# Optimization experiments

Hardware: AMD Instinct MI355X
Metric: run time of the kernel (lower is better)

The kernel has to match this reference:

```python
import jax, jax.numpy as jnp
import numpy as np

EPS = 1e-06
N_HEADS = 32
HEAD_DIM = 128
D_STATE = 128
D_MODEL = 2048
D_INNER = 4096
BATCH = 64


def setup_inputs() -> dict:
    key = jax.random.key(0)
    ks = jax.random.split(key, 8)
    bc_dim = N_HEADS * D_STATE
    theta_dim = N_HEADS * (D_STATE // 2)
    proj_dim = 2 * D_INNER + 2 * bc_dim + 2 * N_HEADS + theta_dim  # 18496
    x = jax.random.normal(ks[0], (BATCH, D_MODEL), jnp.float32)
    h = jax.random.normal(ks[1], (BATCH, N_HEADS, D_STATE, HEAD_DIM), jnp.float32) * 0.1
    B_prev = jax.random.normal(ks[2], (BATCH, N_HEADS, D_STATE), jnp.float32)
    x_prev = jax.random.normal(ks[3], (BATCH, N_HEADS, HEAD_DIM), jnp.float32)
    theta_cumsum = jax.random.normal(ks[4], (BATCH, N_HEADS, D_STATE // 2), jnp.float32)
    W_in = jax.random.normal(ks[5], (proj_dim, D_MODEL), jnp.float32) * 0.02
    # A_log initialized as log(arange(1, d_state+1)) repeated per head
    A_log = jnp.log(jnp.arange(1, D_STATE + 1, dtype=jnp.float32))[None, :].repeat(N_HEADS, axis=0)
    B_bias = jnp.ones((N_HEADS, D_STATE), jnp.float32)
    C_bias = jnp.ones((N_HEADS, D_STATE), jnp.float32)
    W_out = jax.random.normal(ks[6], (D_MODEL, D_INNER), jnp.float32) * 0.02
    return {"x": x, "h": h, "B_prev": B_prev, "x_prev": x_prev,
            "theta_cumsum": theta_cumsum, "W_in": W_in, "A_log": A_log,
            "B_bias": B_bias, "C_bias": C_bias, "W_out": W_out}


def _rms_norm(v):
    # RMS over last dim (v already fp32)
    rms = jnp.sqrt(jnp.mean(v * v, axis=-1, keepdims=True) + EPS)
    return v / rms


def _apply_rope(v, freqs):
    # v: (B,H,N), freqs: (B,H,N//2); interleaved pairs
    vp = v.reshape(*v.shape[:-1], -1, 2)
    c, s = jnp.cos(freqs), jnp.sin(freqs)
    v0, v1 = vp[..., 0], vp[..., 1]
    y0 = v0 * c - v1 * s
    y1 = v0 * s + v1 * c
    return jnp.stack([y0, y1], axis=-1).reshape(v.shape)


def reference(x, h, B_prev, x_prev, theta_cumsum, W_in, A_log, B_bias, C_bias, W_out):
    batch = x.shape[0]
    bc_dim = N_HEADS * D_STATE
    proj = x @ W_in.T  # (B, proj_dim)
    idx = 0
    x_proj = proj[:, idx:idx + D_INNER]; idx += D_INNER
    z = proj[:, idx:idx + D_INNER]; idx += D_INNER
    B_raw = proj[:, idx:idx + bc_dim]; idx += bc_dim
    C_raw = proj[:, idx:idx + bc_dim]; idx += bc_dim
    dt_raw = proj[:, idx:idx + N_HEADS]; idx += N_HEADS
    lam_raw = proj[:, idx:idx + N_HEADS]; idx += N_HEADS
    theta = proj[:, idx:].reshape(batch, N_HEADS, D_STATE // 2)

    x_proj = x_proj.reshape(batch, N_HEADS, HEAD_DIM)
    z = z.reshape(batch, N_HEADS, HEAD_DIM)
    B_raw = B_raw.reshape(batch, N_HEADS, D_STATE)
    C_raw = C_raw.reshape(batch, N_HEADS, D_STATE)

    B = _rms_norm(B_raw) + B_bias
    C = _rms_norm(C_raw) + C_bias

    dt = jax.nn.softplus(dt_raw)                       # (B,H)
    theta_cumsum_new = theta_cumsum + theta * dt[:, :, None]
    B = _apply_rope(B, theta_cumsum_new)
    C = _apply_rope(C, theta_cumsum_new)

    lam = jax.nn.sigmoid(lam_raw)                      # (B,H)
    A = -jnp.mean(jnp.exp(A_log), axis=-1)             # (H,)
    alpha = jnp.exp(dt * A)                            # (B,H)
    beta = (1.0 - lam) * dt * alpha
    gamma = lam * dt

    Bx_prev = jnp.einsum('bhn,bhp->bhnp', B_prev, x_prev)
    Bx_curr = jnp.einsum('bhn,bhp->bhnp', B, x_proj)
    h_new = (alpha[:, :, None, None] * h
             + beta[:, :, None, None] * Bx_prev
             + gamma[:, :, None, None] * Bx_curr)      # (B,H,N,P)

    y = jnp.einsum('bhn,bhnp->bhp', C, h_new)
    y = y * jax.nn.silu(z)
    y = y.reshape(batch, D_INNER) @ W_out.T            # (B, d_model)
    return y, h_new, B, x_proj, theta_cumsum_new
```

## Files before the change

### kernel.cpp

```cpp
#include <hip/hip_runtime.h>
#include <hip/hip_bf16.h>
#include <cstdint>
#include <cmath>

#define EPSV 1e-6f
#define PSTR 1183744

typedef __attribute__((ext_vector_type(8))) short bf16x8;
typedef __attribute__((ext_vector_type(4))) float f32x4;

typedef __attribute__((address_space(3))) unsigned int lds_u32;
typedef const __attribute__((address_space(1))) unsigned int g_u32;

__device__ __forceinline__ void load_lds16(const void* g, void* l) {
  __builtin_amdgcn_global_load_lds((g_u32*)g, (lds_u32*)l, 16, 0, 0);
}

__device__ __forceinline__ short f2b(float f) {
  unsigned u = __float_as_uint(f);
  u = (u + 0x7fffu + ((u >> 16) & 1u)) >> 16;
  return (short)u;
}

__device__ __forceinline__ bf16x8 cvt8(float4 a, float4 b) {
  bf16x8 v;
  v[0]=f2b(a.x); v[1]=f2b(a.y); v[2]=f2b(a.z); v[3]=f2b(a.w);
  v[4]=f2b(b.x); v[5]=f2b(b.y); v[6]=f2b(b.z); v[7]=f2b(b.w);
  return v;
}

__global__ __launch_bounds__(256) void conv_bf16(
    const float* __restrict__ in, short* __restrict__ out, int n8) {
  const int i = blockIdx.x * 256 + threadIdx.x;
  if (i < n8) {
    float4 a = ((const float4*)in)[2 * i];
    float4 b = ((const float4*)in)[2 * i + 1];
    ((bf16x8*)out)[i] = cvt8(a, b);
  }
}

template<int KSPLIT, int NT>
__global__ __launch_bounds__(256, 2) void gemm_wlds(
    const short* __restrict__ Abf, const float* __restrict__ W,
    float* __restrict__ Outp, int N, int K) {
  __shared__ float Wlds[3][64 * 64];
  __shared__ short Alds[3][64 * 64];
  const int tid = threadIdx.x;
  const int lane = tid & 63;
  const int wv = tid >> 6;
  const int lrow = lane & 15, lk = lane >> 4;
  const int bid = blockIdx.x;
  const int ks = bid % KSPLIT;
  const int nblk = (bid / KSPLIT) * 64;
  const int kbase = ks * (NT * 64);

  f32x4 acc[4];
#pragma unroll
  for (int i = 0; i < 4; ++i) acc[i] = (f32x4){0.f, 0.f, 0.f, 0.f};

  auto stage = [&](int buf, int k0) {
#pragma unroll
    for (int j = 0; j < 4; ++j) {
      const int c = wv * 4 + j;
      const int r = c * 4 + (lane >> 4);
      const int g = (lane & 15) ^ (r & 15);
      load_lds16(W + (size_t)(nblk + r) * K + k0 + g * 4,
                 (char*)&Wlds[buf][0] + c * 1024);
    }
#pragma unroll
    for (int j = 0; j < 2; ++j) {
      const int c = wv * 2 + j;
      const int r = c * 8 + (lane >> 3);
      const int g = (lane & 7) ^ (r & 7);
      load_lds16(Abf + (size_t)r * K + k0 + g * 8,
                 (char*)&Alds[buf][0] + c * 1024);
    }
  };

  auto compute = [&](int buf) {
    const int wr = wv * 16 + lrow;
#pragma unroll
    for (int kc = 0; kc < 2; ++kc) {
      const int g0 = kc * 8 + lk * 2;
      const float4 wlo = *(const float4*)((const char*)&Wlds[buf][0]
                          + wr * 256 + ((g0 ^ (lrow & 15)) * 16));
      const float4 whi = *(const float4*)((const char*)&Wlds[buf][0]
                          + wr * 256 + (((g0 + 1) ^ (lrow & 15)) * 16));
      const bf16x8 wb = cvt8(wlo, whi);
#pragma unroll
      for (int mf = 0; mf < 4; ++mf) {
        const int ar = mf * 16 + lrow;
        const int ga = ((kc << 2) | lk) ^ (ar & 7);
        const bf16x8 av = *(const bf16x8*)((const char*)&Alds[buf][0]
                           + ar * 128 + ga * 16);
        acc[mf] = __builtin_amdgcn_mfma_f32_16x16x32_bf16(av, wb, acc[mf], 0, 0, 0);
      }
    }
  };

  stage(0, kbase);
  stage(1, kbase + 64);

  for (int t = 0; t < NT; ++t) {
    if (t < NT - 1) asm volatile("s_waitcnt vmcnt(6)" ::: "memory");
    else            asm volatile("s_waitcnt vmcnt(0)" ::: "memory");
    __builtin_amdgcn_sched_barrier(0);
    __builtin_amdgcn_s_barrier();
    __builtin_amdgcn_sched_barrier(0);
    compute(t % 3);
    if (t + 2 <= NT - 1) stage((t + 2) % 3, kbase + (t + 2) * 64);
  }

  float* ob = Outp + (size_t)ks * 64 * N + nblk + wv * 16 + lrow;
#pragma unroll
  for (int mf = 0; mf < 4; ++mf)
#pragma unroll
    for (int i = 0; i < 4; ++i)
      ob[(size_t)(mf * 16 + lk * 4 + i) * N] = acc[mf][i];
}

__device__ __forceinline__ float block_reduce_sum256(float v, float* red, int t) {
#pragma unroll
  for (int o = 32; o > 0; o >>= 1) v += __shfl_xor(v, o, 64);
  __syncthreads();
  if ((t & 63) == 0) red[t >> 6] = v;
  __syncthreads();
  return red[0] + red[1] + red[2] + red[3];
}

__global__ __launch_bounds__(256) void state_update(
    const float* __restrict__ pp, const float* __restrict__ h,
    const float* __restrict__ B_prev, const float* __restrict__ x_prev,
    const float* __restrict__ theta_cumsum, const float* __restrict__ A_log,
    const float* __restrict__ B_bias, const float* __restrict__ C_bias,
    float* __restrict__ o_h, float* __restrict__ o_B,
    float* __restrict__ o_xp, float* __restrict__ o_th,
    short* __restrict__ ysbf) {
  const int bid = blockIdx.x;
  const int b = bid >> 5, hd = bid & 31;
  const int t = threadIdx.x;
  const size_t pb = (size_t)b * 18496;
#define PJ(o) (pp[pb + (o)] + pp[PSTR + pb + (o)] + pp[2 * PSTR + pb + (o)] \
             + pp[3 * PSTR + pb + (o)])

  __shared__ float sB[128], sC[128], sBp[128], sXp[128], sXv[128];
  __shared__ float red[8];
  __shared__ float yred[8][128];

  float aval = (t < 128) ? expf(A_log[hd * 128 + t]) : 0.f;
  float brv  = (t < 128) ? PJ(8192 + hd * 128 + t) : 0.f;
  float crv  = (t < 128) ? PJ(12288 + hd * 128 + t) : 0.f;
  if (t < 128) {
    sBp[t] = B_prev[(size_t)bid * 128 + t];
    float xp = PJ(hd * 128 + t);
    sXp[t] = xp;
    o_xp[(size_t)bid * 128 + t] = xp;
    sXv[t] = x_prev[(size_t)bid * 128 + t];
  }
  float sumA  = block_reduce_sum256(aval, red, t);
  float sumB2 = block_reduce_sum256(brv * brv, red, t);
  float sumC2 = block_reduce_sum256(crv * crv, red, t);

  const float dt_raw  = PJ(16384 + hd);
  const float lam_raw = PJ(16416 + hd);
  const float dt  = (dt_raw > 20.f) ? dt_raw : log1pf(expf(dt_raw));
  const float lam = 1.f / (1.f + expf(-lam_raw));
  const float A     = -sumA * (1.f / 128.f);
  const float alpha = expf(dt * A);
  const float beta  = (1.f - lam) * dt * alpha;
  const float gamma = lam * dt;
  const float rb = rsqrtf(sumB2 * (1.f / 128.f) + EPSV);
  const float rc = rsqrtf(sumC2 * (1.f / 128.f) + EPSV);

  if (t < 64) {
    float b0 = PJ(8192 + hd * 128 + 2 * t);
    float b1 = PJ(8192 + hd * 128 + 2 * t + 1);
    float c0 = PJ(12288 + hd * 128 + 2 * t);
    float c1 = PJ(12288 + hd * 128 + 2 * t + 1);
    b0 = b0 * rb + B_bias[hd * 128 + 2 * t];
    b1 = b1 * rb + B_bias[hd * 128 + 2 * t + 1];
    c0 = c0 * rc + C_bias[hd * 128 + 2 * t];
    c1 = c1 * rc + C_bias[hd * 128 + 2 * t + 1];
    const float th = theta_cumsum[(size_t)bid * 64 + t]
                   + PJ(16448 + hd * 64 + t) * dt;
    o_th[(size_t)bid * 64 + t] = th;
    const float cth = cosf(th), sth = sinf(th);
    const float nb0 = b0 * cth - b1 * sth, nb1 = b0 * sth + b1 * cth;
    const float nc0 = c0 * cth - c1 * sth, nc1 = c0 * sth + c1 * cth;
    sB[2 * t] = nb0; sB[2 * t + 1] = nb1;
    sC[2 * t] = nc0; sC[2 * t + 1] = nc1;
    o_B[(size_t)bid * 128 + 2 * t] = nb0;
    o_B[(size_t)bid * 128 + 2 * t + 1] = nb1;
  }
  __syncthreads();

  const int p4 = t & 31, nb = t >> 5;
  const float4 xp4 = *(const float4*)&sXp[p4 * 4];
  const float4 xv4 = *(const float4*)&sXv[p4 * 4];
  const size_t hbase = (size_t)bid * 16384;
  float4 ya = {0.f, 0.f, 0.f, 0.f};
  for (int n = nb; n < 128; n += 8) {
    const float4 hv = *(const float4*)&h[hbase + n * 128 + p4 * 4];
    const float cb = gamma * sB[n];
    const float cp = beta * sBp[n];
    float4 hn;
    hn.x = alpha * hv.x + cp * xv4.x + cb * xp4.x;
    hn.y = alpha * hv.y + cp * xv4.y + cb * xp4.y;
    hn.z = alpha * hv.z + cp * xv4.z + cb * xp4.z;
    hn.w = alpha * hv.w + cp * xv4.w + cb * xp4.w;
    *(float4*)&o_h[hbase + n * 128 + p4 * 4] = hn;
    const float cn = sC[n];
    ya.x += cn * hn.x; ya.y += cn * hn.y; ya.z += cn * hn.z; ya.w += cn * hn.w;
  }
  *(float4*)&yred[nb][p4 * 4] = ya;
  __syncthreads();
  if (t < 128) {
    float y = 0.f;
#pragma unroll
    for (int j = 0; j < 8; ++j) y += yred[j][t];
    const float zv = PJ(4096 + hd * 128 + t);
    const float sig = 1.f / (1.f + expf(-zv));
    ysbf[(size_t)b * 4096 + hd * 128 + t] = f2b(y * zv * sig);
  }
#undef PJ
}

__global__ __launch_bounds__(256) void reduce_y(
    const float* __restrict__ yp, float* __restrict__ y, int n4) {
  const int i = blockIdx.x * 256 + threadIdx.x;
  if (i < n4) {
    float4 s = ((const float4*)yp)[i];
#pragma unroll
    for (int k = 1; k < 16; ++k) {
      float4 t = ((const float4*)(yp + (size_t)k * 131072))[i];
      s.x += t.x; s.y += t.y; s.z += t.z; s.w += t.w;
    }
    ((float4*)y)[i] = s;
  }
}

extern "C" void kernel_launch(void* const* d_in, const int* in_sizes, int n_in,
                              void* d_out, int out_size, void* d_ws, size_t ws_size,
                              hipStream_t stream) {
  const float* x            = (const float*)d_in[0];
  const float* h            = (const float*)d_in[1];
  const float* B_prev       = (const float*)d_in[2];
  const float* x_prev       = (const float*)d_in[3];
  const float* theta_cumsum = (const float*)d_in[4];
  const float* W_in         = (const float*)d_in[5];
  const float* A_log        = (const float*)d_in[6];
  const float* B_bias       = (const float*)d_in[7];
  const float* C_bias       = (const float*)d_in[8];
  const float* W_out        = (const float*)d_in[9];

  float* out  = (float*)d_out;
  float* o_y  = out;
  float* o_h  = out + 131072;
  float* o_B  = o_h + 33554432;
  float* o_xp = o_B + 262144;
  float* o_th = o_xp + 262144;

  float* pp   = (float*)d_ws;
  float* yp   = pp;
  short* xbf  = (short*)(pp + 4 * PSTR);
  short* ysbf = xbf + 131072;

  conv_bf16<<<dim3(64), dim3(256), 0, stream>>>(x, xbf, 16384);
  gemm_wlds<4, 8><<<dim3(289 * 4), dim3(256), 0, stream>>>(
      xbf, W_in, pp, 18496, 2048);
  state_update<<<dim3(2048), dim3(256), 0, stream>>>(
      pp, h, B_prev, x_prev, theta_cumsum, A_log, B_bias, C_bias,
      o_h, o_B, o_xp, o_th, ysbf);
  gemm_wlds<16, 4><<<dim3(32 * 16), dim3(256), 0, stream>>>(
      ysbf, W_out, yp, 2048, 4096);
  reduce_y<<<dim3(128), dim3(256), 0, stream>>>(yp, o_y, 32768);
}
```

Baseline: 121.1 us.

## Shrink GEMM tiles to 32 wide and cut K-split partials

Replaces the 64x64-tile GEMM with a 32-column, 32-deep K-step variant that uses less LDS per block and raises the occupancy hint to 6 blocks per CU. The K-split drops from 4 to 2 for the input projection and from 16 to 8 for the output projection, so state_update sums two partial buffers instead of four and reduce_y sums eight. The aim is to cut partial-sum traffic and improve latency hiding through more resident blocks. The cost is more loop iterations, each doing less MFMA work, which may expose barrier and load overhead. The state-update inner loop also gets an unroll-4 pragma.

```diff
diff --git a/kernel.cpp b/kernel.cpp
--- a/kernel.cpp
+++ b/kernel.cpp
@@ -40,83 +40,74 @@
 }
 
 template<int KSPLIT, int NT>
-__global__ __launch_bounds__(256, 2) void gemm_wlds(
+__global__ __launch_bounds__(256, 6) void gemm_t32(
     const short* __restrict__ Abf, const float* __restrict__ W,
     float* __restrict__ Outp, int N, int K) {
-  __shared__ float Wlds[3][64 * 64];
-  __shared__ short Alds[3][64 * 64];
+  __shared__ float Wlds[3][32 * 32];
+  __shared__ short Alds[3][64 * 32];
   const int tid = threadIdx.x;
   const int lane = tid & 63;
   const int wv = tid >> 6;
   const int lrow = lane & 15, lk = lane >> 4;
   const int bid = blockIdx.x;
   const int ks = bid % KSPLIT;
-  const int nblk = (bid / KSPLIT) * 64;
-  const int kbase = ks * (NT * 64);
-
-  f32x4 acc[4];
-#pragma unroll
-  for (int i = 0; i < 4; ++i) acc[i] = (f32x4){0.f, 0.f, 0.f, 0.f};
+  const int nblk = (bid / KSPLIT) * 32;
+  const int kbase = ks * (NT * 32);
+
+  f32x4 acc[2];
+  acc[0] = (f32x4){0.f, 0.f, 0.f, 0.f};
+  acc[1] = (f32x4){0.f, 0.f, 0.f, 0.f};
 
   auto stage = [&](int buf, int k0) {
-#pragma unroll
-    for (int j = 0; j < 4; ++j) {
-      const int c = wv * 4 + j;
-      const int r = c * 4 + (lane >> 4);
-      const int g = (lane & 15) ^ (r & 15);
+    {
+      const int r = wv * 8 + (lane >> 3);
+      const int g = (lane & 7) ^ (r & 7);
       load_lds16(W + (size_t)(nblk + r) * K + k0 + g * 4,
-                 (char*)&Wlds[buf][0] + c * 1024);
-    }
-#pragma unroll
-    for (int j = 0; j < 2; ++j) {
-      const int c = wv * 2 + j;
-      const int r = c * 8 + (lane >> 3);
-      const int g = (lane & 7) ^ (r & 7);
+                 (char*)&Wlds[buf][0] + wv * 1024);
+    }
+    {
+      const int r = wv * 16 + (lane >> 2);
+      const int g = (lane & 3) ^ (r & 3);
       load_lds16(Abf + (size_t)r * K + k0 + g * 8,
-                 (char*)&Alds[buf][0] + c * 1024);
+                 (char*)&Alds[buf][0] + wv * 1024);
     }
   };
 
   auto compute = [&](int buf) {
-    const int wr = wv * 16 + lrow;
-#pragma unroll
-    for (int kc = 0; kc < 2; ++kc) {
-      const int g0 = kc * 8 + lk * 2;
-      const float4 wlo = *(const float4*)((const char*)&Wlds[buf][0]
-                          + wr * 256 + ((g0 ^ (lrow & 15)) * 16));
-      const float4 whi = *(const float4*)((const char*)&Wlds[buf][0]
-                          + wr * 256 + (((g0 + 1) ^ (lrow & 15)) * 16));
-      const bf16x8 wb = cvt8(wlo, whi);
-#pragma unroll
-      for (int mf = 0; mf < 4; ++mf) {
-        const int ar = mf * 16 + lrow;
-        const int ga = ((kc << 2) | lk) ^ (ar & 7);
-        const bf16x8 av = *(const bf16x8*)((const char*)&Alds[buf][0]
-                           + ar * 128 + ga * 16);
-        acc[mf] = __builtin_amdgcn_mfma_f32_16x16x32_bf16(av, wb, acc[mf], 0, 0, 0);
-      }
+    const int rn = (wv & 1) * 16 + lrow;
+    const float4 wlo = *(const float4*)((const char*)&Wlds[buf][0]
+                        + rn * 128 + (((2 * lk)     ^ (rn & 7)) * 16));
+    const float4 whi = *(const float4*)((const char*)&Wlds[buf][0]
+                        + rn * 128 + (((2 * lk + 1) ^ (rn & 7)) * 16));
+    const bf16x8 wb = cvt8(wlo, whi);
+#pragma unroll
+    for (int mf = 0; mf < 2; ++mf) {
+      const int ar = (wv >> 1) * 32 + mf * 16 + lrow;
+      const bf16x8 av = *(const bf16x8*)((const char*)&Alds[buf][0]
+                         + ar * 64 + ((lk ^ (ar & 3)) * 16));
+      acc[mf] = __builtin_amdgcn_mfma_f32_16x16x32_bf16(av, wb, acc[mf], 0, 0, 0);
     }
   };
 
   stage(0, kbase);
-  stage(1, kbase + 64);
+  stage(1, kbase + 32);
 
   for (int t = 0; t < NT; ++t) {
-    if (t < NT - 1) asm volatile("s_waitcnt vmcnt(6)" ::: "memory");
+    if (t < NT - 1) asm volatile("s_waitcnt vmcnt(2)" ::: "memory");
     else            asm volatile("s_waitcnt vmcnt(0)" ::: "memory");
     __builtin_amdgcn_sched_barrier(0);
     __builtin_amdgcn_s_barrier();
     __builtin_amdgcn_sched_barrier(0);
     compute(t % 3);
-    if (t + 2 <= NT - 1) stage((t + 2) % 3, kbase + (t + 2) * 64);
-  }
-
-  float* ob = Outp + (size_t)ks * 64 * N + nblk + wv * 16 + lrow;
-#pragma unroll
-  for (int mf = 0; mf < 4; ++mf)
+    if (t + 2 <= NT - 1) stage((t + 2) % 3, kbase + (t + 2) * 32);
+  }
+
+  float* ob = Outp + (size_t)ks * 64 * N + nblk + (wv & 1) * 16 + lrow;
+#pragma unroll
+  for (int mf = 0; mf < 2; ++mf)
 #pragma unroll
     for (int i = 0; i < 4; ++i)
-      ob[(size_t)(mf * 16 + lk * 4 + i) * N] = acc[mf][i];
+      ob[(size_t)((wv >> 1) * 32 + mf * 16 + lk * 4 + i) * N] = acc[mf][i];
 }
 
 __device__ __forceinline__ float block_reduce_sum256(float v, float* red, int t) {
@@ -129,7 +120,8 @@
 }
 
 __global__ __launch_bounds__(256) void state_update(
-    const float* __restrict__ pp, const float* __restrict__ h,
+    const float* __restrict__ pp0, const float* __restrict__ pp1,
+    const float* __restrict__ h,
     const float* __restrict__ B_prev, const float* __restrict__ x_prev,
     const float* __restrict__ theta_cumsum, const float* __restrict__ A_log,
     const float* __restrict__ B_bias, const float* __restrict__ C_bias,
@@ -140,8 +132,7 @@
   const int b = bid >> 5, hd = bid & 31;
   const int t = threadIdx.x;
   const size_t pb = (size_t)b * 18496;
-#define PJ(o) (pp[pb + (o)] + pp[PSTR + pb + (o)] + pp[2 * PSTR + pb + (o)] \
-             + pp[3 * PSTR + pb + (o)])
+#define PJ(o) (pp0[pb + (o)] + pp1[pb + (o)])
 
   __shared__ float sB[128], sC[128], sBp[128], sXp[128], sXv[128];
   __shared__ float red[8];
@@ -199,6 +190,7 @@
   const float4 xv4 = *(const float4*)&sXv[p4 * 4];
   const size_t hbase = (size_t)bid * 16384;
   float4 ya = {0.f, 0.f, 0.f, 0.f};
+#pragma unroll 4
   for (int n = nb; n < 128; n += 8) {
     const float4 hv = *(const float4*)&h[hbase + n * 128 + p4 * 4];
     const float cb = gamma * sB[n];
@@ -231,7 +223,7 @@
   if (i < n4) {
     float4 s = ((const float4*)yp)[i];
 #pragma unroll
-    for (int k = 1; k < 16; ++k) {
+    for (int k = 1; k < 8; ++k) {
       float4 t = ((const float4*)(yp + (size_t)k * 131072))[i];
       s.x += t.x; s.y += t.y; s.z += t.z; s.w += t.w;
     }
@@ -262,16 +254,16 @@
 
   float* pp   = (float*)d_ws;
   float* yp   = pp;
-  short* xbf  = (short*)(pp + 4 * PSTR);
+  short* xbf  = (short*)(pp + 2 * PSTR);
   short* ysbf = xbf + 131072;
 
   conv_bf16<<<dim3(64), dim3(256), 0, stream>>>(x, xbf, 16384);
-  gemm_wlds<4, 8><<<dim3(289 * 4), dim3(256), 0, stream>>>(
+  gemm_t32<2, 32><<<dim3(578 * 2), dim3(256), 0, stream>>>(
       xbf, W_in, pp, 18496, 2048);
   state_update<<<dim3(2048), dim3(256), 0, stream>>>(
-      pp, h, B_prev, x_prev, theta_cumsum, A_log, B_bias, C_bias,
+      pp, pp + PSTR, h, B_prev, x_prev, theta_cumsum, A_log, B_bias, C_bias,
       o_h, o_B, o_xp, o_th, ysbf);
-  gemm_wlds<16, 4><<<dim3(32 * 16), dim3(256), 0, stream>>>(
+  gemm_t32<8, 16><<<dim3(64 * 8), dim3(256), 0, stream>>>(
       ysbf, W_out, yp, 2048, 4096);
   reduce_y<<<dim3(128), dim3(256), 0, stream>>>(yp, o_y, 32768);
 }
```

Measured after the change: 126.1 us. 1.04x slower.
